# Kernel optimization log

Measured on AMD Instinct MI355X. Metric: run time of the kernel, lower is better.

The kernel has to match this reference:

```python
import jax, jax.numpy as jnp
import numpy as np
from jax import lax

NUM_HEADS = 8
EPS_BN = 1e-5
EPS_LN = 1e-5


def setup_inputs() -> dict:
    key = jax.random.key(0)
    ks = iter(jax.random.split(key, 32))
    C = 512
    R = C // 16  # channel-gate reduction
    HID = 512    # classifier hidden
    NC = 1       # num_classes

    def gn(shape, scale=0.02):
        return (jax.random.normal(next(ks), shape, dtype=jnp.float32) * scale)

    inp = {
        "x": jax.random.normal(next(ks), (16, C, 28, 28), dtype=jnp.float32),
        # ChannelGate MLP (Linear(C,R) -> ReLU -> Linear(R,C))
        "mlp_w1": gn((R, C)), "mlp_b1": jnp.zeros((R,), jnp.float32),
        "mlp_w2": gn((C, R)), "mlp_b2": jnp.zeros((C,), jnp.float32),
        # SpatialGate 7x7 conv (2->1, no bias) + BatchNorm2d(1) eval-mode stats
        "sp_w": gn((1, 2, 7, 7)),
        "sp_gamma": jnp.ones((1,), jnp.float32), "sp_beta": jnp.zeros((1,), jnp.float32),
        "sp_mean": jnp.zeros((1,), jnp.float32), "sp_var": jnp.ones((1,), jnp.float32),
        # attention projections
        "wq": gn((C, C)), "bq": jnp.zeros((C,), jnp.float32),
        "wk": gn((C, C)), "bk": jnp.zeros((C,), jnp.float32),
        "wv": gn((C, C)), "bv": jnp.zeros((C,), jnp.float32),
        "wo": gn((C, C)), "bo": jnp.zeros((C,), jnp.float32),
        # classifier: LayerNorm(C) -> Linear(C,512) -> ReLU -> Linear(512,NC)
        "ln_g": jnp.ones((C,), jnp.float32), "ln_b": jnp.zeros((C,), jnp.float32),
        "fc1_w": gn((HID, C)), "fc1_b": jnp.zeros((HID,), jnp.float32),
        "fc2_w": gn((NC, HID)), "fc2_b": jnp.zeros((NC,), jnp.float32),
    }
    return inp


def reference(x, mlp_w1, mlp_b1, mlp_w2, mlp_b2, sp_w, sp_gamma, sp_beta,
              sp_mean, sp_var, wq, bq, wk, bk, wv, bv, wo, bo,
              ln_g, ln_b, fc1_w, fc1_b, fc2_w, fc2_b):
    B, C, H, W = x.shape
    N = H * W
    hd = C // NUM_HEADS

    # ---- CBAM: channel gate (avg + max global pools through shared MLP) ----
    def mlp(p):  # p: [B, C]
        return jax.nn.relu(p @ mlp_w1.T + mlp_b1) @ mlp_w2.T + mlp_b2

    avg_p = x.mean(axis=(2, 3))
    max_p = x.max(axis=(2, 3))
    ch_scale = jax.nn.sigmoid(mlp(avg_p) + mlp(max_p))[:, :, None, None]
    x = x * ch_scale

    # ---- CBAM: spatial gate ----
    comp = jnp.concatenate([x.max(axis=1, keepdims=True),
                            x.mean(axis=1, keepdims=True)], axis=1)  # [B,2,H,W]
    s = lax.conv_general_dilated(comp, sp_w, window_strides=(1, 1),
                                 padding=[(3, 3), (3, 3)],
                                 dimension_numbers=("NCHW", "OIHW", "NCHW"))
    s = (s - sp_mean[None, :, None, None]) * lax.rsqrt(sp_var + EPS_BN)[None, :, None, None]
    s = s * sp_gamma[None, :, None, None] + sp_beta[None, :, None, None]
    x = x * jax.nn.sigmoid(s)

    # ---- multi-head self-attention over HW tokens ----
    xf = x.reshape(B, C, N).transpose(0, 2, 1)  # [B, N, C]

    def heads(w, b):
        return (xf @ w.T + b).reshape(B, N, NUM_HEADS, hd).transpose(0, 2, 1, 3)

    Q, K, V = heads(wq, bq), heads(wk, bk), heads(wv, bv)  # [B, h, N, d]
    scores = jnp.einsum("bhnd,bhmd->bhnm", Q, K) / jnp.sqrt(jnp.float32(hd))
    attn = jax.nn.softmax(scores, axis=-1)  # dropout is identity in eval
    attended = jnp.einsum("bhnm,bhmd->bhnd", attn, V)
    attended = attended.transpose(0, 2, 1, 3).reshape(B, N, C)
    attended = attended @ wo.T + bo
    x = x + attended.transpose(0, 2, 1).reshape(B, C, H, W)

    # ---- classifier head ----
    p = x.mean(axis=(2, 3))  # AdaptiveAvgPool2d(1) + Flatten -> [B, C]
    mu = p.mean(axis=-1, keepdims=True)
    var = p.var(axis=-1, keepdims=True)
    ln = (p - mu) * lax.rsqrt(var + EPS_LN) * ln_g + ln_b
    h = jax.nn.relu(ln @ fc1_w.T + fc1_b)
    return h @ fc2_w.T + fc2_b
```

## Files before the change

kernel.cpp:

```cpp
#include <hip/hip_runtime.h>
#include <math.h>

#define BB 16
#define CC 512
#define HW 784
#define RR 32
#define NHD 8
#define HD 64
#define NT 784
#define NTILE 49
#define CBS 131

#define OFS_AVGP   0
#define OFS_MAXP   8192
#define OFS_CHS    16384
#define OFS_CMAX   24576
#define OFS_CMEAN  37120
#define OFS_SP     49664
#define OFS_P1     62208
#define OFS_ABAR   70400
#define OFS_XG     78592
#define XG_SZ      (BB*CC*HW)
#define OFS_XGT    (OFS_XG + XG_SZ)
#define OFS_QBF    (OFS_XGT + XG_SZ/2)
#define OFS_KBF    (OFS_QBF + XG_SZ/2)
#define OFS_V2     (OFS_KBF + XG_SZ/2)
#define OFS_WF     (OFS_V2 + XG_SZ)
#define OFS_W      OFS_XG
#define OFS_PV     (OFS_XG + 131072)
#define OFS_LNV    (OFS_PV + 8192)
#define OFS_H1     (OFS_LNV + 8192)
#define OFS_CMAXP  (OFS_XG + 262144)
#define OFS_CMEANP (OFS_CMAXP + 200704)

typedef __attribute__((ext_vector_type(8))) short bf16x8;
typedef __attribute__((ext_vector_type(4))) float f32x4;

__device__ __forceinline__ unsigned short f2bf(float x) {
  union { float f; unsigned u; } v; v.f = x;
  unsigned r = v.u + 0x7fffu + ((v.u >> 16) & 1u);
  return (unsigned short)(r >> 16);
}
__device__ __forceinline__ float bf2f(unsigned short x) {
  union { unsigned u; float f; } v; v.u = ((unsigned)x) << 16;
  return v.f;
}

__global__ void k_pool(const float* __restrict__ x, float* avg_p, float* max_p) {
  int wid = threadIdx.x >> 6;
  int lane = threadIdx.x & 63;
  int row = blockIdx.x * 4 + wid;
  const float* xr = x + (size_t)row * HW;
  float s = 0.f, m = -INFINITY;
  for (int i = lane; i < HW; i += 64) { float v = xr[i]; s += v; m = fmaxf(m, v); }
  for (int o = 32; o; o >>= 1) { s += __shfl_down(s, o, 64); m = fmaxf(m, __shfl_down(m, o, 64)); }
  if (lane == 0) { avg_p[row] = s * (1.f/HW); max_p[row] = m; }
}

__global__ void k_chmlp(const float* avg_p, const float* max_p,
                        const float* w1, const float* b1,
                        const float* w2, const float* b2, float* chs) {
  __shared__ float pa[CC], pm[CC], part[256], hr[64];
  int b = blockIdx.x, t = threadIdx.x;
  for (int i = t; i < CC; i += 256) { pa[i] = avg_p[b*CC+i]; pm[i] = max_p[b*CC+i]; }
  __syncthreads();
  {
    int rp = t & 63, ch = t >> 6;
    int r = rp & 31;
    const float* src = (rp < 32) ? pa : pm;
    const float* wr = w1 + (size_t)r*CC + ch*128;
    float s = 0.f;
    #pragma unroll 8
    for (int c = 0; c < 128; c++) s += src[ch*128 + c] * wr[c];
    part[t] = s;
  }
  __syncthreads();
  if (t < 64)
    hr[t] = fmaxf(part[t] + part[64+t] + part[128+t] + part[192+t] + b1[t & 31], 0.f);
  __syncthreads();
  for (int c = t; c < CC; c += 256) {
    float a = 2.f*b2[c];
    const float* wr = w2 + c*RR;
    #pragma unroll
    for (int r = 0; r < RR; r++) a += (hr[r]+hr[32+r])*wr[r];
    chs[b*CC+c] = 1.f/(1.f+__expf(-a));
  }
}

__global__ void k_chgatep(const float* __restrict__ x, const float* __restrict__ chs,
                          float* __restrict__ cmaxp, float* __restrict__ cmeanp) {
  __shared__ float cs[32];
  int b = blockIdx.x, cg = blockIdx.y, t = threadIdx.x;
  if (t < 32) cs[t] = chs[b*CC + cg*32 + t];
  __syncthreads();
  const float* xb = x + ((size_t)b*CC + cg*32)*HW;
  for (int pix = t; pix < HW; pix += 256) {
    float mx = -INFINITY, sm = 0.f;
    #pragma unroll
    for (int c = 0; c < 32; c++) {
      float v = xb[(size_t)c*HW + pix] * cs[c];
      mx = fmaxf(mx, v); sm += v;
    }
    cmaxp[(size_t)(cg*BB + b)*HW + pix] = mx;
    cmeanp[(size_t)(cg*BB + b)*HW + pix] = sm;
  }
}

__global__ void k_credsp(const float* __restrict__ cmaxp, const float* __restrict__ cmeanp,
                         const float* __restrict__ w, const float* g, const float* be,
                         const float* mu, const float* var, float* __restrict__ sp) {
  __shared__ float cmx[HW], cmn[HW];
  int b = blockIdx.x, t = threadIdx.x;
  for (int pix = t; pix < HW; pix += 256) {
    float mx = -INFINITY, sm = 0.f;
    #pragma unroll
    for (int cg = 0; cg < 16; cg++) {
      mx = fmaxf(mx, cmaxp[(size_t)(cg*BB + b)*HW + pix]);
      sm += cmeanp[(size_t)(cg*BB + b)*HW + pix];
    }
    cmx[pix] = mx; cmn[pix] = sm * (1.f/CC);
  }
  __syncthreads();
  float bnscale = rsqrtf(var[0]+1e-5f)*g[0];
  for (int pix = t; pix < HW; pix += 256) {
    int h = pix/28, wd = pix%28;
    float acc = 0.f;
    for (int kh = 0; kh < 7; kh++) {
      int ih = h + kh - 3; if (ih < 0 || ih >= 28) continue;
      for (int kw = 0; kw < 7; kw++) {
        int iw = wd + kw - 3; if (iw < 0 || iw >= 28) continue;
        int ip = ih*28+iw;
        acc += cmx[ip]*w[kh*7+kw] + cmn[ip]*w[49+kh*7+kw];
      }
    }
    float s = (acc - mu[0])*bnscale + be[0];
    sp[b*HW+pix] = 1.f/(1.f+__expf(-s));
  }
}

__global__ void k_sfuse(const float* __restrict__ x, const float* __restrict__ chs,
                        const float* __restrict__ sp, unsigned short* __restrict__ xgT,
                        float* __restrict__ p1) {
  __shared__ float cs[CC];
  int nt = blockIdx.x, b = blockIdx.y;
  int t = threadIdx.x, ln = t & 63;
  for (int i = t; i < CC; i += 256) cs[i] = chs[b*CC+i];
  __syncthreads();
  int n = nt*16 + (ln & 15);
  float spv = sp[b*HW + n];
  const float* xb = x + (size_t)b*CC*HW;
  #pragma unroll
  for (int i = 0; i < 4; i++) {
    int s = (t >> 6) + 4*i;
    int c = s*32 + (ln >> 4)*8;
    float v[8]; bf16x8 p;
    #pragma unroll
    for (int j = 0; j < 8; j++) {
      v[j] = xb[(size_t)(c+j)*HW + n] * cs[c+j] * spv;
      p[j] = (short)f2bf(v[j]);
    }
    *(bf16x8*)(xgT + ((((size_t)b*NTILE + nt)*16 + s)*64 + ln)*8) = p;
    #pragma unroll
    for (int j = 0; j < 8; j++) {
      float sv = v[j];
      sv += __shfl_xor(sv, 1, 64); sv += __shfl_xor(sv, 2, 64);
      sv += __shfl_xor(sv, 4, 64); sv += __shfl_xor(sv, 8, 64);
      if ((ln & 15) == 0) atomicAdd(&p1[b*CC + c + j], sv * (1.f/HW));
    }
  }
}

__global__ void k_wfrag(const float* __restrict__ wq, const float* __restrict__ wk,
                        const float* __restrict__ wv, unsigned short* __restrict__ Wf) {
  int idx = blockIdx.x*256 + threadIdx.x;
  int ln = idx & 63;
  int s  = (idx >> 6) & 15;
  int ct = (idx >> 10) & 31;
  int mat = idx >> 15;
  const float* W = (mat==0)? wq : (mat==1)? wk : wv;
  const float* src = W + (size_t)(ct*16 + (ln & 15))*CC + s*32 + (ln >> 4)*8;
  float4 f0 = *(const float4*)src;
  float4 f1 = *(const float4*)(src + 4);
  bf16x8 p;
  p[0]=(short)f2bf(f0.x); p[1]=(short)f2bf(f0.y); p[2]=(short)f2bf(f0.z); p[3]=(short)f2bf(f0.w);
  p[4]=(short)f2bf(f1.x); p[5]=(short)f2bf(f1.y); p[6]=(short)f2bf(f1.z); p[7]=(short)f2bf(f1.w);
  *(bf16x8*)(Wf + (size_t)idx*8) = p;
}

__global__ __launch_bounds__(256) void k_qkv_mfma(
    const unsigned short* __restrict__ xgT, const unsigned short* __restrict__ Wf,
    const float* __restrict__ bq, const float* __restrict__ bk, const float* __restrict__ bv,
    unsigned short* __restrict__ Qbf, unsigned short* __restrict__ Kbf,
    unsigned short* __restrict__ Vbf) {
  __shared__ float Cb[64*CBS];
  int blk = blockIdx.x;
  int yb = blk / 208;
  int r0 = blk % 208;
  int mt = r0 >> 4;
  int b  = r0 & 15;
  int mat = yb >> 2;
  int c0 = (yb & 3) * 128;
  int t = threadIdx.x, w = t >> 6, ln = t & 63;
  const unsigned short* Ab = xgT + (size_t)b*NTILE*8192;
  const unsigned short* Bb = Wf + (size_t)mat*32*8192;
  int ctg0 = (c0 >> 4) + w*2;
  f32x4 acc[4][2];
  #pragma unroll
  for (int m = 0; m < 4; m++)
    #pragma unroll
    for (int c2 = 0; c2 < 2; c2++) acc[m][c2] = (f32x4){0.f,0.f,0.f,0.f};
  int ntc[4];
  #pragma unroll
  for (int m = 0; m < 4; m++) { int nt = 4*mt + m; ntc[m] = (nt > 48) ? 48 : nt; }
  #pragma unroll 2
  for (int s = 0; s < 16; s++) {
    bf16x8 bf0 = *(const bf16x8*)(Bb + (size_t)(ctg0*16 + s)*512 + ln*8);
    bf16x8 bf1 = *(const bf16x8*)(Bb + (size_t)((ctg0+1)*16 + s)*512 + ln*8);
    bf16x8 af[4];
    #pragma unroll
    for (int m = 0; m < 4; m++)
      af[m] = *(const bf16x8*)(Ab + (size_t)(ntc[m]*16 + s)*512 + ln*8);
    #pragma unroll
    for (int m = 0; m < 4; m++) {
      acc[m][0] = __builtin_amdgcn_mfma_f32_16x16x32_bf16(af[m], bf0, acc[m][0], 0,0,0);
      acc[m][1] = __builtin_amdgcn_mfma_f32_16x16x32_bf16(af[m], bf1, acc[m][1], 0,0,0);
    }
  }
  #pragma unroll
  for (int m = 0; m < 4; m++)
    #pragma unroll
    for (int c2 = 0; c2 < 2; c2++)
      #pragma unroll
      for (int r = 0; r < 4; r++)
        Cb[(m*16 + (ln>>4)*4 + r)*CBS + w*32 + c2*16 + (ln&15)] = acc[m][c2][r];
  __syncthreads();
  const float* bias = (mat==0)? bq : (mat==1)? bk : bv;
  #pragma unroll
  for (int i = 0; i < 4; i++) {
    int p = w*4 + i;
    int ntl = p >> 2, sl = p & 3;
    int nt = 4*mt + ntl;
    if (nt > 48) continue;
    int row = ntl*16 + (ln & 15);
    int col = sl*32 + (ln >> 4)*8;
    float v[8];
    #pragma unroll
    for (int j = 0; j < 8; j++) v[j] = Cb[row*CBS + col + j] + bias[c0 + col + j];
    int token = nt*16 + (ln & 15);
    int h = (c0 >> 6) + (sl >> 1);
    int bh = b*NHD + h;
    bf16x8 pk;
    #pragma unroll
    for (int j = 0; j < 8; j++) pk[j] = (short)f2bf(v[j]);
    if (mat < 2) {
      unsigned short* Out = (mat == 0) ? Qbf : Kbf;
      *(bf16x8*)(Out + ((size_t)bh*NTILE + nt)*1024 + (size_t)(sl & 1)*512 + ln*8) = pk;
    } else {
      int d = (sl & 1)*32 + (ln >> 4)*8;
      *(bf16x8*)(Vbf + ((size_t)bh*NT + token)*HD + d) = pk;
    }
  }
}

__global__ __launch_bounds__(256, 5) void k_attn7(const unsigned short* __restrict__ Qbf,
    const unsigned short* __restrict__ Kbf, float* __restrict__ wsum) {
  __shared__ float l_tmp[64];
  __shared__ float rl[16];
  int bh = blockIdx.x & 127, nt = blockIdx.x >> 7;
  int t = threadIdx.x, w = t >> 6, ln = t & 63;
  const unsigned short* Qb = Qbf + ((size_t)bh*NTILE + nt)*1024;
  const unsigned short* Kb = Kbf + (size_t)bh*NTILE*1024;
  bf16x8 q0 = *(const bf16x8*)(Qb + ln*8);
  bf16x8 q1 = *(const bf16x8*)(Qb + 512 + ln*8);
  f32x4 ev[13];
  float lp[4] = {0.f,0.f,0.f,0.f};
  #pragma unroll
  for (int i = 0; i < 13; i++) {
    int mt = w + 4*i;
    bool valid = (i < 12) || (w == 0);
    int mtc = valid ? mt : 48;
    bf16x8 k0 = *(const bf16x8*)(Kb + (size_t)mtc*1024 + ln*8);
    bf16x8 k1 = *(const bf16x8*)(Kb + (size_t)mtc*1024 + 512 + ln*8);
    f32x4 a = {0.f,0.f,0.f,0.f};
    a = __builtin_amdgcn_mfma_f32_16x16x32_bf16(q0, k0, a, 0,0,0);
    a = __builtin_amdgcn_mfma_f32_16x16x32_bf16(q1, k1, a, 0,0,0);
    f32x4 e;
    #pragma unroll
    for (int r = 0; r < 4; r++) e[r] = __expf(a[r]*0.125f);
    ev[i] = e;
    if (valid) {
      #pragma unroll
      for (int r = 0; r < 4; r++) lp[r] += e[r];
    }
  }
  #pragma unroll
  for (int r = 0; r < 4; r++) {
    float v = lp[r];
    v += __shfl_xor(v,1,64); v += __shfl_xor(v,2,64);
    v += __shfl_xor(v,4,64); v += __shfl_xor(v,8,64);
    if ((ln & 15) == 0) l_tmp[w*16 + (ln>>4)*4 + r] = v;
  }
  __syncthreads();
  if (t < 16) rl[t] = 1.f / (l_tmp[t] + l_tmp[16+t] + l_tmp[32+t] + l_tmp[48+t]);
  __syncthreads();
  f32x4 rlq = *(const f32x4*)&rl[(ln >> 4)*4];
  #pragma unroll
  for (int i = 0; i < 13; i++) {
    int mt = w + 4*i;
    bool valid = (i < 12) || (w == 0);
    float v = ev[i][0]*rlq[0] + ev[i][1]*rlq[1] + ev[i][2]*rlq[2] + ev[i][3]*rlq[3];
    v += __shfl_xor(v, 16, 64);
    v += __shfl_xor(v, 32, 64);
    if (valid && ln < 16)
      atomicAdd(&wsum[bh*NT + mt*16 + ln], v);
  }
}

__global__ void k_attn_av(const float* __restrict__ w, const unsigned short* __restrict__ Vm,
                          float* __restrict__ abar) {
  __shared__ float red[256];
  int bh = blockIdx.x, t = threadIdx.x;
  int d = t & 63, chunk = t >> 6;
  float acc = 0.f;
  const unsigned short* vb = Vm + (size_t)bh*NT*HD;
  const float* wb = w + bh*NT;
  for (int m = chunk*196; m < (chunk+1)*196; m++)
    acc += wb[m] * bf2f(vb[(size_t)m*HD + d]);
  red[t] = acc;
  __syncthreads();
  if (t < 64)
    abar[bh*HD + t] = (red[t] + red[64+t] + red[128+t] + red[192+t]) * (1.f/NT);
}

__global__ void k_headA(const float* __restrict__ p1, const float* __restrict__ abar,
                        const float* __restrict__ wo, const float* __restrict__ bo,
                        float* __restrict__ pv) {
  int b = blockIdx.x, cg = blockIdx.y;
  int t = threadIdx.x, w = t >> 6, ln = t & 63;
  float a[8];
  #pragma unroll
  for (int k = 0; k < 8; k++) a[k] = abar[b*CC + ln + 64*k];
  int c0 = cg*64 + w*16;
  for (int i = 0; i < 16; i++) {
    int c = c0 + i;
    const float* wr = wo + (size_t)c*CC;
    float s = 0.f;
    #pragma unroll
    for (int k = 0; k < 8; k++) s += a[k] * wr[ln + 64*k];
    for (int o = 32; o; o >>= 1) s += __shfl_down(s, o, 64);
    if (ln == 0) pv[b*CC + c] = s + bo[c] + p1[b*CC + c];
  }
}

__global__ void k_headB(const float* __restrict__ pv, const float* __restrict__ ln_g,
                        const float* __restrict__ ln_b, float* __restrict__ lnv) {
  int b = blockIdx.x, ln = threadIdx.x;
  float v[8], s = 0.f, s2 = 0.f;
  #pragma unroll
  for (int k = 0; k < 8; k++) { v[k] = pv[b*CC + ln + 64*k]; s += v[k]; s2 += v[k]*v[k]; }
  for (int o = 32; o; o >>= 1) { s += __shfl_down(s, o, 64); s2 += __shfl_down(s2, o, 64); }
  s = __shfl(s, 0, 64); s2 = __shfl(s2, 0, 64);
  float mean = s * (1.f/CC);
  float rs = rsqrtf(s2*(1.f/CC) - mean*mean + 1e-5f);
  #pragma unroll
  for (int k = 0; k < 8; k++) {
    int c = ln + 64*k;
    lnv[b*CC + c] = (v[k]-mean)*rs*ln_g[c] + ln_b[c];
  }
}

__global__ void k_headC(const float* __restrict__ lnv, const float* __restrict__ fc1_w,
                        const float* __restrict__ fc1_b, float* __restrict__ h1) {
  int b = blockIdx.x, cg = blockIdx.y;
  int t = threadIdx.x, w = t >> 6, ln = t & 63;
  float a[8];
  #pragma unroll
  for (int k = 0; k < 8; k++) a[k] = lnv[b*CC + ln + 64*k];
  int c0 = cg*64 + w*16;
  for (int i = 0; i < 16; i++) {
    int c = c0 + i;
    const float* wr = fc1_w + (size_t)c*CC;
    float s = 0.f;
    #pragma unroll
    for (int k = 0; k < 8; k++) s += a[k] * wr[ln + 64*k];
    for (int o = 32; o; o >>= 1) s += __shfl_down(s, o, 64);
    if (ln == 0) h1[b*CC + c] = fmaxf(s + fc1_b[c], 0.f);
  }
}

__global__ void k_headD(const float* __restrict__ h1, const float* __restrict__ fc2_w,
                        const float* __restrict__ fc2_b, float* __restrict__ out) {
  int b = blockIdx.x, ln = threadIdx.x;
  float s = 0.f;
  #pragma unroll
  for (int k = 0; k < 8; k++) s += h1[b*CC + ln + 64*k] * fc2_w[ln + 64*k];
  for (int o = 32; o; o >>= 1) s += __shfl_down(s, o, 64);
  if (ln == 0) out[b] = s + fc2_b[0];
}

extern "C" void kernel_launch(void* const* d_in, const int* in_sizes, int n_in,
                              void* d_out, int out_size, void* d_ws, size_t ws_size,
                              hipStream_t stream) {
  const float* x       = (const float*)d_in[0];
  const float* mlp_w1  = (const float*)d_in[1];
  const float* mlp_b1  = (const float*)d_in[2];
  const float* mlp_w2  = (const float*)d_in[3];
  const float* mlp_b2  = (const float*)d_in[4];
  const float* sp_w    = (const float*)d_in[5];
  const float* sp_g    = (const float*)d_in[6];
  const float* sp_b    = (const float*)d_in[7];
  const float* sp_mu   = (const float*)d_in[8];
  const float* sp_var  = (const float*)d_in[9];
  const float* wq      = (const float*)d_in[10];
  const float* bq      = (const float*)d_in[11];
  const float* wk      = (const float*)d_in[12];
  const float* bk      = (const float*)d_in[13];
  const float* wv      = (const float*)d_in[14];
  const float* bv      = (const float*)d_in[15];
  const float* wo      = (const float*)d_in[16];
  const float* bo      = (const float*)d_in[17];
  const float* ln_g    = (const float*)d_in[18];
  const float* ln_b    = (const float*)d_in[19];
  const float* fc1_w   = (const float*)d_in[20];
  const float* fc1_b   = (const float*)d_in[21];
  const float* fc2_w   = (const float*)d_in[22];
  const float* fc2_b   = (const float*)d_in[23];

  float* ws = (float*)d_ws;
  float* avg_p = ws + OFS_AVGP;
  float* max_p = ws + OFS_MAXP;
  float* chs   = ws + OFS_CHS;
  float* sp    = ws + OFS_SP;
  float* p1    = ws + OFS_P1;
  float* abar  = ws + OFS_ABAR;
  unsigned short* xgT = (unsigned short*)(ws + OFS_XGT);
  unsigned short* Qbf = (unsigned short*)(ws + OFS_QBF);
  unsigned short* Kbf = (unsigned short*)(ws + OFS_KBF);
  unsigned short* Vbf = (unsigned short*)(ws + OFS_V2);
  unsigned short* Wf  = (unsigned short*)(ws + OFS_WF);
  float* wsum  = ws + OFS_W;
  float* pv    = ws + OFS_PV;
  float* lnv   = ws + OFS_LNV;
  float* h1    = ws + OFS_H1;
  float* cmaxp = ws + OFS_CMAXP;
  float* cmeanp= ws + OFS_CMEANP;

  hipMemsetAsync(p1, 0, BB*CC*sizeof(float), stream);
  hipMemsetAsync(wsum, 0, BB*NHD*NT*sizeof(float), stream);

  k_pool   <<<2048, 256, 0, stream>>>(x, avg_p, max_p);
  k_chmlp  <<<BB, 256, 0, stream>>>(avg_p, max_p, mlp_w1, mlp_b1, mlp_w2, mlp_b2, chs);
  k_chgatep<<<dim3(BB,16), 256, 0, stream>>>(x, chs, cmaxp, cmeanp);
  k_credsp <<<BB, 256, 0, stream>>>(cmaxp, cmeanp, sp_w, sp_g, sp_b, sp_mu, sp_var, sp);
  k_wfrag  <<<384, 256, 0, stream>>>(wq, wk, wv, Wf);
  k_sfuse  <<<dim3(NTILE,BB), 256, 0, stream>>>(x, chs, sp, xgT, p1);
  k_qkv_mfma<<<2496, 256, 0, stream>>>(xgT, Wf, bq, bk, bv, Qbf, Kbf, Vbf);
  k_attn7  <<<NTILE*128, 256, 0, stream>>>(Qbf, Kbf, wsum);
  k_attn_av<<<128, 256, 0, stream>>>(wsum, Vbf, abar);
  k_headA  <<<dim3(BB,8), 256, 0, stream>>>(p1, abar, wo, bo, pv);
  k_headB  <<<BB, 64, 0, stream>>>(pv, ln_g, ln_b, lnv);
  k_headC  <<<dim3(BB,8), 256, 0, stream>>>(lnv, fc1_w, fc1_b, h1);
  k_headD  <<<BB, 64, 0, stream>>>(h1, fc2_w, fc2_b, (float*)d_out);
}
```

Baseline: 291.8 us.

## Replace atomic pooling with separate reduction kernel, fuse LayerNorm into fc1, vectorize LDS reads

New measurement: 273.1 us. 1.07x faster.

```diff
diff --git a/kernel.cpp b/kernel.cpp
--- a/kernel.cpp
+++ b/kernel.cpp
@@ -9,13 +9,11 @@
 #define HD 64
 #define NT 784
 #define NTILE 49
-#define CBS 131
+#define CBS 132
 
 #define OFS_AVGP   0
 #define OFS_MAXP   8192
 #define OFS_CHS    16384
-#define OFS_CMAX   24576
-#define OFS_CMEAN  37120
 #define OFS_SP     49664
 #define OFS_P1     62208
 #define OFS_ABAR   70400
@@ -28,8 +26,7 @@
 #define OFS_WF     (OFS_V2 + XG_SZ)
 #define OFS_W      OFS_XG
 #define OFS_PV     (OFS_XG + 131072)
-#define OFS_LNV    (OFS_PV + 8192)
-#define OFS_H1     (OFS_LNV + 8192)
+#define OFS_H1     (OFS_PV + 8192)
 #define OFS_CMAXP  (OFS_XG + 262144)
 #define OFS_CMEANP (OFS_CMAXP + 200704)
 
@@ -139,8 +136,7 @@
 }
 
 __global__ void k_sfuse(const float* __restrict__ x, const float* __restrict__ chs,
-                        const float* __restrict__ sp, unsigned short* __restrict__ xgT,
-                        float* __restrict__ p1) {
+                        const float* __restrict__ sp, unsigned short* __restrict__ xgT) {
   __shared__ float cs[CC];
   int nt = blockIdx.x, b = blockIdx.y;
   int t = threadIdx.x, ln = t & 63;
@@ -153,21 +149,34 @@
   for (int i = 0; i < 4; i++) {
     int s = (t >> 6) + 4*i;
     int c = s*32 + (ln >> 4)*8;
-    float v[8]; bf16x8 p;
-    #pragma unroll
-    for (int j = 0; j < 8; j++) {
-      v[j] = xb[(size_t)(c+j)*HW + n] * cs[c+j] * spv;
-      p[j] = (short)f2bf(v[j]);
-    }
+    bf16x8 p;
+    #pragma unroll
+    for (int j = 0; j < 8; j++)
+      p[j] = (short)f2bf(xb[(size_t)(c+j)*HW + n] * cs[c+j] * spv);
     *(bf16x8*)(xgT + ((((size_t)b*NTILE + nt)*16 + s)*64 + ln)*8) = p;
-    #pragma unroll
-    for (int j = 0; j < 8; j++) {
-      float sv = v[j];
-      sv += __shfl_xor(sv, 1, 64); sv += __shfl_xor(sv, 2, 64);
-      sv += __shfl_xor(sv, 4, 64); sv += __shfl_xor(sv, 8, 64);
-      if ((ln & 15) == 0) atomicAdd(&p1[b*CC + c + j], sv * (1.f/HW));
-    }
-  }
+  }
+}
+
+__global__ void k_p1(const unsigned short* __restrict__ xgT, float* __restrict__ p1) {
+  __shared__ float red[4][32];
+  int b = blockIdx.x, s = blockIdx.y;
+  int t = threadIdx.x, w = t >> 6, ln = t & 63;
+  float acc[8] = {0.f,0.f,0.f,0.f,0.f,0.f,0.f,0.f};
+  for (int nt = w; nt < NTILE; nt += 4) {
+    bf16x8 p = *(const bf16x8*)(xgT + ((((size_t)b*NTILE + nt)*16 + s)*64 + ln)*8);
+    #pragma unroll
+    for (int j = 0; j < 8; j++) acc[j] += bf2f((unsigned short)p[j]);
+  }
+  #pragma unroll
+  for (int j = 0; j < 8; j++) {
+    float v = acc[j];
+    v += __shfl_xor(v,1,64); v += __shfl_xor(v,2,64);
+    v += __shfl_xor(v,4,64); v += __shfl_xor(v,8,64);
+    if ((ln & 15) == 0) red[w][(ln>>4)*8 + j] = v;
+  }
+  __syncthreads();
+  if (t < 32)
+    p1[b*CC + s*32 + t] = (red[0][t]+red[1][t]+red[2][t]+red[3][t]) * (1.f/HW);
 }
 
 __global__ void k_wfrag(const float* __restrict__ wq, const float* __restrict__ wk,
@@ -192,7 +201,7 @@
     const float* __restrict__ bq, const float* __restrict__ bk, const float* __restrict__ bv,
     unsigned short* __restrict__ Qbf, unsigned short* __restrict__ Kbf,
     unsigned short* __restrict__ Vbf) {
-  __shared__ float Cb[64*CBS];
+  __shared__ __align__(16) float Cb[64*CBS];
   int blk = blockIdx.x;
   int yb = blk / 208;
   int r0 = blk % 208;
@@ -243,9 +252,11 @@
     if (nt > 48) continue;
     int row = ntl*16 + (ln & 15);
     int col = sl*32 + (ln >> 4)*8;
-    float v[8];
-    #pragma unroll
-    for (int j = 0; j < 8; j++) v[j] = Cb[row*CBS + col + j] + bias[c0 + col + j];
+    float4 v0 = *(const float4*)&Cb[row*CBS + col];
+    float4 v1 = *(const float4*)&Cb[row*CBS + col + 4];
+    float v[8] = {v0.x, v0.y, v0.z, v0.w, v1.x, v1.y, v1.z, v1.w};
+    #pragma unroll
+    for (int j = 0; j < 8; j++) v[j] += bias[c0 + col + j];
     int token = nt*16 + (ln & 15);
     int h = (c0 >> 6) + (sl >> 1);
     int bh = b*NHD + h;
@@ -262,7 +273,7 @@
   }
 }
 
-__global__ __launch_bounds__(256, 5) void k_attn7(const unsigned short* __restrict__ Qbf,
+__global__ __launch_bounds__(256, 4) void k_attn7(const unsigned short* __restrict__ Qbf,
     const unsigned short* __restrict__ Kbf, float* __restrict__ wsum) {
   __shared__ float l_tmp[64];
   __shared__ float rl[16];
@@ -352,39 +363,34 @@
   }
 }
 
-__global__ void k_headB(const float* __restrict__ pv, const float* __restrict__ ln_g,
-                        const float* __restrict__ ln_b, float* __restrict__ lnv) {
-  int b = blockIdx.x, ln = threadIdx.x;
-  float v[8], s = 0.f, s2 = 0.f;
-  #pragma unroll
-  for (int k = 0; k < 8; k++) { v[k] = pv[b*CC + ln + 64*k]; s += v[k]; s2 += v[k]*v[k]; }
+__global__ void k_headC(const float* __restrict__ pv, const float* __restrict__ ln_g,
+                        const float* __restrict__ ln_b, const float* __restrict__ fc1_w,
+                        const float* __restrict__ fc1_b, float* __restrict__ h1) {
+  int b = blockIdx.x, cg = blockIdx.y;
+  int t = threadIdx.x, w = t >> 6, ln = t & 63;
+  float a[8];
+  float s = 0.f, s2 = 0.f;
+  #pragma unroll
+  for (int k = 0; k < 8; k++) {
+    a[k] = pv[b*CC + ln + 64*k];
+    s += a[k]; s2 += a[k]*a[k];
+  }
   for (int o = 32; o; o >>= 1) { s += __shfl_down(s, o, 64); s2 += __shfl_down(s2, o, 64); }
   s = __shfl(s, 0, 64); s2 = __shfl(s2, 0, 64);
   float mean = s * (1.f/CC);
   float rs = rsqrtf(s2*(1.f/CC) - mean*mean + 1e-5f);
   #pragma unroll
-  for (int k = 0; k < 8; k++) {
-    int c = ln + 64*k;
-    lnv[b*CC + c] = (v[k]-mean)*rs*ln_g[c] + ln_b[c];
-  }
-}
-
-__global__ void k_headC(const float* __restrict__ lnv, const float* __restrict__ fc1_w,
-                        const float* __restrict__ fc1_b, float* __restrict__ h1) {
-  int b = blockIdx.x, cg = blockIdx.y;
-  int t = threadIdx.x, w = t >> 6, ln = t & 63;
-  float a[8];
-  #pragma unroll
-  for (int k = 0; k < 8; k++) a[k] = lnv[b*CC + ln + 64*k];
+  for (int k = 0; k < 8; k++)
+    a[k] = (a[k]-mean)*rs*ln_g[ln + 64*k] + ln_b[ln + 64*k];
   int c0 = cg*64 + w*16;
   for (int i = 0; i < 16; i++) {
     int c = c0 + i;
     const float* wr = fc1_w + (size_t)c*CC;
-    float s = 0.f;
-    #pragma unroll
-    for (int k = 0; k < 8; k++) s += a[k] * wr[ln + 64*k];
-    for (int o = 32; o; o >>= 1) s += __shfl_down(s, o, 64);
-    if (ln == 0) h1[b*CC + c] = fmaxf(s + fc1_b[c], 0.f);
+    float v = 0.f;
+    #pragma unroll
+    for (int k = 0; k < 8; k++) v += a[k] * wr[ln + 64*k];
+    for (int o = 32; o; o >>= 1) v += __shfl_down(v, o, 64);
+    if (ln == 0) h1[b*CC + c] = fmaxf(v + fc1_b[c], 0.f);
   }
 }
 
@@ -440,12 +446,10 @@
   unsigned short* Wf  = (unsigned short*)(ws + OFS_WF);
   float* wsum  = ws + OFS_W;
   float* pv    = ws + OFS_PV;
-  float* lnv   = ws + OFS_LNV;
   float* h1    = ws + OFS_H1;
   float* cmaxp = ws + OFS_CMAXP;
   float* cmeanp= ws + OFS_CMEANP;
 
-  hipMemsetAsync(p1, 0, BB*CC*sizeof(float), stream);
   hipMemsetAsync(wsum, 0, BB*NHD*NT*sizeof(float), stream);
 
   k_pool   <<<2048, 256, 0, stream>>>(x, avg_p, max_p);
@@ -453,12 +457,12 @@
   k_chgatep<<<dim3(BB,16), 256, 0, stream>>>(x, chs, cmaxp, cmeanp);
   k_credsp <<<BB, 256, 0, stream>>>(cmaxp, cmeanp, sp_w, sp_g, sp_b, sp_mu, sp_var, sp);
   k_wfrag  <<<384, 256, 0, stream>>>(wq, wk, wv, Wf);
-  k_sfuse  <<<dim3(NTILE,BB), 256, 0, stream>>>(x, chs, sp, xgT, p1);
+  k_sfuse  <<<dim3(NTILE,BB), 256, 0, stream>>>(x, chs, sp, xgT);
+  k_p1     <<<dim3(BB,16), 256, 0, stream>>>(xgT, p1);
   k_qkv_mfma<<<2496, 256, 0, stream>>>(xgT, Wf, bq, bk, bv, Qbf, Kbf, Vbf);
   k_attn7  <<<NTILE*128, 256, 0, stream>>>(Qbf, Kbf, wsum);
   k_attn_av<<<128, 256, 0, stream>>>(wsum, Vbf, abar);
   k_headA  <<<dim3(BB,8), 256, 0, stream>>>(p1, abar, wo, bo, pv);
-  k_headB  <<<BB, 64, 0, stream>>>(pv, ln_g, ln_b, lnv);
-  k_headC  <<<dim3(BB,8), 256, 0, stream>>>(lnv, fc1_w, fc1_b, h1);
+  k_headC  <<<dim3(BB,8), 256, 0, stream>>>(pv, ln_g, ln_b, fc1_w, fc1_b, h1);
   k_headD  <<<BB, 64, 0, stream>>>(h1, fc2_w, fc2_b, (float*)d_out);
 }
```
